# Kernel optimization log

Hardware: AMD Instinct MI355X
Metric: run time of the kernel (lower is better)

## Reference

```python
import jax, jax.numpy as jnp
import numpy as np

B, N, CIN, COUT = 2, 150000, 64, 64
SPATIAL = (128, 128, 128)  # spatial_shape forward arg, fixed here (list arg)
EPS = 1e-5


def setup_inputs() -> dict:
    key = jax.random.key(0)
    k1, k2, k3 = jax.random.split(key, 3)
    features = jax.random.normal(k1, (B, N, CIN), jnp.float32)
    coordinates = jax.random.randint(k2, (B, N, 3), 0, SPATIAL[0], jnp.int32)
    # SparseConv3d weight: 3x3x3 kernel flattened to 27 offsets, [27, Cin, Cout]
    weight = jax.random.normal(k3, (27, CIN, COUT), jnp.float32) * 0.05
    gamma = jnp.ones((COUT,), jnp.float32)
    beta = jnp.zeros((COUT,), jnp.float32)
    return {"features": features, "coordinates": coordinates, "weight": weight,
            "gamma": gamma, "beta": beta, "batch_size": B}


def _rulebook_ids(coordinates, batch_size):
    """For each of 27 kernel offsets, the flat input-point id feeding each output
    site (output sites = input sites, rulebook gather). Empty/OOB -> BN (zero row)."""
    X, Y, Z = SPATIAL
    Np = coordinates.shape[1]
    BN = batch_size * Np
    pid = jnp.arange(BN, dtype=jnp.int32)
    b = jnp.repeat(jnp.arange(batch_size, dtype=jnp.int32), Np)
    c = coordinates.reshape(-1, 3)
    # dense voxel hash: coord -> point id (max for deterministic collision handling)
    grid = jnp.full((batch_size, X, Y, Z), -1, jnp.int32)
    grid = grid.at[b, c[:, 0], c[:, 1], c[:, 2]].max(pid)
    # 27 offsets in {-1,0,1}^3 (padding=1, kernel=3, stride=1)
    r = jnp.arange(-1, 2, dtype=jnp.int32)
    offs = jnp.stack(jnp.meshgrid(r, r, r, indexing="ij"), -1).reshape(27, 3)
    nc = c[None, :, :] + offs[:, None, :]                      # [27, BN, 3]
    hi = jnp.array([X, Y, Z], jnp.int32)
    valid = jnp.all((nc >= 0) & (nc < hi), axis=-1)            # [27, BN]
    ncc = jnp.clip(nc, 0, hi - 1)
    ids = grid[b[None, :], ncc[..., 0], ncc[..., 1], ncc[..., 2]]
    return jnp.where(valid & (ids >= 0), ids, BN)              # BN -> zero row


def reference(features, coordinates, weight, gamma, beta, batch_size):
    Bs, Np, Cin = features.shape
    BN = Bs * Np
    ids = _rulebook_ids(coordinates, batch_size)               # [27, BN]
    feats = jnp.concatenate(
        [features.reshape(BN, Cin), jnp.zeros((1, Cin), features.dtype)], 0)

    # gather-GEMM-scatter accumulated over the 27 kernel offsets
    def step(acc, xs):
        idk, wk = xs
        return acc + feats[idk] @ wk, None

    out0 = jnp.zeros((BN, weight.shape[-1]), features.dtype)
    out, _ = jax.lax.scan(step, out0, (ids, weight))

    # BatchNorm1d (training stats over all points) + ReLU
    mean = out.mean(axis=0)
    var = out.var(axis=0)
    out = (out - mean) * jax.lax.rsqrt(var + EPS) * gamma + beta
    out = jax.nn.relu(out)
    return out.reshape(Bs, Np, -1)
```

## Files before the change

kernel.cpp:

```cpp
#include <hip/hip_runtime.h>

#define GS 128
#define GS3 (GS*GS*GS)
#define NPTS 150000
#define NBATCH 2
#define BN_TOT (NBATCH*NPTS)
#define CONV_BLOCKS 2344
#define BN_PAD (CONV_BLOCKS*128)
#define ZROW   BN_PAD
#define EPS 1e-5f
#define NBKT 8192

#define OFF_GRID   0ull
#define SZ_GRID    ((size_t)NBATCH*GS3*4)
#define OFF_WFRAG  (OFF_GRID + SZ_GRID)
#define SZ_WFRAG   ((size_t)27*4096*2)
#define OFF_STATS  (OFF_WFRAG + SZ_WFRAG)
#define OFF_CNT    (OFF_STATS + 512)
#define OFF_CUR    (OFF_CNT + NBKT*4)
#define OFF_SIDX   (OFF_CUR + NBKT*4)
#define OFF_CSORT  (OFF_SIDX + 1200128)
#define OFF_FB16S  (OFF_CSORT + (size_t)BN_PAD*16)
#define OFF_IDS    (OFF_FB16S + (size_t)(BN_PAD+1)*128)

typedef __attribute__((ext_vector_type(8))) short bf16x8;
typedef __attribute__((ext_vector_type(4))) float f32x4;
typedef unsigned int u32;
typedef const __attribute__((address_space(1))) u32* gas_u32p;
typedef __attribute__((address_space(3))) u32* las_u32p;

__device__ __forceinline__ short f2bf(float f) {
    union { float f; unsigned u; } v; v.f = f;
    unsigned rr = v.u + 0x7fffu + ((v.u >> 16) & 1u);
    return (short)(rr >> 16);
}

__global__ __launch_bounds__(256) void k_count(const int* __restrict__ coords,
                                               int* __restrict__ grid,
                                               u32* __restrict__ cnt) {
    int p = blockIdx.x*256 + threadIdx.x;
    if (p >= BN_TOT) return;
    int x = coords[p*3+0], y = coords[p*3+1], z = coords[p*3+2];
    int b = (p >= NPTS);
    atomicMax(&grid[(b<<21) | (x<<14) | (y<<7) | z], p);
    atomicAdd(&cnt[(b<<12) | ((x>>3)<<8) | ((y>>3)<<4) | (z>>3)], 1u);
}

__global__ __launch_bounds__(1024) void k_scan(const u32* __restrict__ cnt,
                                               u32* __restrict__ cur) {
    __shared__ u32 ps[1024];
    int t = threadIdx.x;
    u32 l[8]; u32 s = 0;
    #pragma unroll
    for (int i = 0; i < 8; ++i) { l[i] = cnt[t*8+i]; s += l[i]; }
    ps[t] = s; __syncthreads();
    for (int off = 1; off < 1024; off <<= 1) {
        u32 v = (t >= off) ? ps[t-off] : 0u; __syncthreads();
        ps[t] += v; __syncthreads();
    }
    u32 run = (t == 0) ? 0u : ps[t-1];
    #pragma unroll
    for (int i = 0; i < 8; ++i) { cur[t*8+i] = run; run += l[i]; }
}

__global__ __launch_bounds__(256) void k_place(const float* __restrict__ feats,
                                               const int* __restrict__ coords,
                                               u32* __restrict__ cur,
                                               int* __restrict__ sortidx,
                                               int4* __restrict__ csorted,
                                               ushort* __restrict__ fb16s) {
    int p = blockIdx.x*256 + threadIdx.x;
    if (p >= BN_PAD) return;
    if (p >= BN_TOT) { csorted[p] = make_int4(-9,-9,-9,0); return; }
    int x = coords[p*3+0], y = coords[p*3+1], z = coords[p*3+2];
    int b = (p >= NPTS);
    int bkt = (b<<12) | ((x>>3)<<8) | ((y>>3)<<4) | (z>>3);
    int pos = (int)atomicAdd(&cur[bkt], 1u);
    sortidx[p] = pos;
    csorted[pos] = make_int4(x, y, z, p);
    const float4* s = (const float4*)(feats + (size_t)p*64);
    ushort* d = fb16s + (size_t)pos*64;
    #pragma unroll
    for (int i = 0; i < 8; ++i) {
        float4 a = s[2*i], c = s[2*i+1];
        ushort4 u0 = { (ushort)f2bf(a.x),(ushort)f2bf(a.y),(ushort)f2bf(a.z),(ushort)f2bf(a.w) };
        ushort4 u1 = { (ushort)f2bf(c.x),(ushort)f2bf(c.y),(ushort)f2bf(c.z),(ushort)f2bf(c.w) };
        ((ushort4*)d)[2*i] = u0; ((ushort4*)d)[2*i+1] = u1;
    }
}

__global__ __launch_bounds__(256) void k_ids(const int4* __restrict__ csorted,
                                             const int* __restrict__ grid,
                                             const int* __restrict__ sortidx,
                                             int* __restrict__ ids) {
    int s = blockIdx.x*256 + threadIdx.x;
    if (s >= BN_PAD) return;
    int4 c = csorted[s];
    const bool pad = (s >= BN_TOT);
    const int gb = (c.w >= NPTS) ? GS3 : 0;
    #pragma unroll
    for (int k = 0; k < 27; ++k) {
        int dx = k/9 - 1, dy = (k/3)%3 - 1, dz = k%3 - 1;
        int nx = c.x+dx, ny = c.y+dy, nz = c.z+dz;
        int sid = ZROW;
        if (!pad && (((unsigned)nx < 128u) & ((unsigned)ny < 128u) &
                     ((unsigned)nz < 128u))) {
            int pid = grid[gb + (nx<<14) + (ny<<7) + nz];
            if (pid >= 0) sid = sortidx[pid];
        }
        ids[(size_t)k*BN_PAD + s] = sid;
    }
}

__global__ __launch_bounds__(256) void k_prefrag(const float* __restrict__ w,
                                                 short* __restrict__ wfrag) {
    int t = blockIdx.x * 256 + threadIdx.x;
    if (t >= 27*2*4*64*8) return;
    int i    = t & 7;
    int lane = (t >> 3) & 63;
    int tt   = (t >> 9) & 3;
    int c    = (t >> 11) & 1;
    int k    = t >> 12;
    int kk = c*32 + (lane >> 4)*8 + i;
    int co = tt*16 + (lane & 15);
    wfrag[t] = f2bf(w[(k*64 + kk)*64 + co]);
}

__global__ __launch_bounds__(256, 3) void k_conv(
    const ushort* __restrict__ fb16s,
    const int4* __restrict__ csorted,
    const int* __restrict__ ids_g,
    const ushort* __restrict__ wfrag,
    float* __restrict__ out,
    float* __restrict__ gstats)
{
    __shared__ __align__(16) ushort ldsB[2][4096];
    __shared__ int ids_lds[27*128];
    __shared__ float bsum[64], bsq[64];

    const int tid  = threadIdx.x;
    const int lane = tid & 63;
    const int wv   = tid >> 6;
    const int r    = lane & 15;
    const int seg  = lane >> 4;
    const int p0b  = blockIdx.x * 128;
    const int wrow = wv*32 + r;

    auto stage = [&](int kk, int bsel) {
        const u32* g = (const u32*)(wfrag + (size_t)kk*4096) + tid*4;
        u32* l  = (u32*)(&ldsB[bsel][wv*512]);
        __builtin_amdgcn_global_load_lds((gas_u32p)g,  (las_u32p)l,  16, 0, 0);
        const u32* g2 = g + 1024;
        u32* l2 = (u32*)(&ldsB[bsel][2048 + wv*512]);
        __builtin_amdgcn_global_load_lds((gas_u32p)g2, (las_u32p)l2, 16, 0, 0);
    };

#define LDA4(AC, sid0, sid1) {                                            \
        const ushort* a0_ = fb16s + (size_t)(sid0)*64 + seg*8;            \
        const ushort* a1_ = fb16s + (size_t)(sid1)*64 + seg*8;            \
        AC[0] = *(const bf16x8*)(a0_);  AC[1] = *(const bf16x8*)(a0_+32); \
        AC[2] = *(const bf16x8*)(a1_);  AC[3] = *(const bf16x8*)(a1_+32); }

    f32x4 t0q0={0,0,0,0}, t0q1={0,0,0,0}, t0q2={0,0,0,0}, t0q3={0,0,0,0};
    f32x4 t1q0={0,0,0,0}, t1q1={0,0,0,0}, t1q2={0,0,0,0}, t1q3={0,0,0,0};
    bf16x8 aE[4], aO[4];

    #pragma unroll
    for (int c = 0; c < 14; ++c) {
        int idx = c*256 + tid;
        if (idx < 27*128)
            ids_lds[idx] = ids_g[(size_t)(idx>>7)*BN_PAD + p0b + (idx&127)];
    }
    int i00 = ids_g[p0b + wrow];
    int i01 = ids_g[p0b + wrow + 16];
    int i10 = ids_g[(size_t)BN_PAD + p0b + wrow];
    int i11 = ids_g[(size_t)BN_PAD + p0b + wrow + 16];
    __syncthreads();
    __builtin_amdgcn_sched_barrier(0);
    LDA4(aE, i00, i01);
    __builtin_amdgcn_sched_barrier(0);
    stage(0, 0);
    __builtin_amdgcn_sched_barrier(0);
    LDA4(aO, i10, i11);
    __builtin_amdgcn_sched_barrier(0);

    auto phase = [&](int k, bf16x8 (&AC)[4], int bsel) {
        asm volatile("s_waitcnt vmcnt(4)" ::: "memory");
        __builtin_amdgcn_sched_barrier(0);
        __builtin_amdgcn_s_barrier();
        __builtin_amdgcn_sched_barrier(0);
        const bf16x8* bb = (const bf16x8*)ldsB[bsel];
        bf16x8 b0 = bb[0*64+lane], b1 = bb[1*64+lane],
               b2 = bb[2*64+lane], b3 = bb[3*64+lane],
               b4 = bb[4*64+lane], b5 = bb[5*64+lane],
               b6 = bb[6*64+lane], b7 = bb[7*64+lane];
        int kp2 = (k+2 > 26) ? 26 : k+2;
        int idn0 = ids_lds[kp2*128 + wrow];
        int idn1 = ids_lds[kp2*128 + wrow + 16];
        if (k < 26) stage(k+1, bsel^1);
        __builtin_amdgcn_sched_barrier(0);
        t0q0 = __builtin_amdgcn_mfma_f32_16x16x32_bf16(AC[0], b0, t0q0, 0,0,0);
        t0q1 = __builtin_amdgcn_mfma_f32_16x16x32_bf16(AC[0], b1, t0q1, 0,0,0);
        t0q2 = __builtin_amdgcn_mfma_f32_16x16x32_bf16(AC[0], b2, t0q2, 0,0,0);
        t0q3 = __builtin_amdgcn_mfma_f32_16x16x32_bf16(AC[0], b3, t0q3, 0,0,0);
        t0q0 = __builtin_amdgcn_mfma_f32_16x16x32_bf16(AC[1], b4, t0q0, 0,0,0);
        t0q1 = __builtin_amdgcn_mfma_f32_16x16x32_bf16(AC[1], b5, t0q1, 0,0,0);
        t0q2 = __builtin_amdgcn_mfma_f32_16x16x32_bf16(AC[1], b6, t0q2, 0,0,0);
        t0q3 = __builtin_amdgcn_mfma_f32_16x16x32_bf16(AC[1], b7, t0q3, 0,0,0);
        t1q0 = __builtin_amdgcn_mfma_f32_16x16x32_bf16(AC[2], b0, t1q0, 0,0,0);
        t1q1 = __builtin_amdgcn_mfma_f32_16x16x32_bf16(AC[2], b1, t1q1, 0,0,0);
        t1q2 = __builtin_amdgcn_mfma_f32_16x16x32_bf16(AC[2], b2, t1q2, 0,0,0);
        t1q3 = __builtin_amdgcn_mfma_f32_16x16x32_bf16(AC[2], b3, t1q3, 0,0,0);
        t1q0 = __builtin_amdgcn_mfma_f32_16x16x32_bf16(AC[3], b4, t1q0, 0,0,0);
        t1q1 = __builtin_amdgcn_mfma_f32_16x16x32_bf16(AC[3], b5, t1q1, 0,0,0);
        t1q2 = __builtin_amdgcn_mfma_f32_16x16x32_bf16(AC[3], b6, t1q2, 0,0,0);
        t1q3 = __builtin_amdgcn_mfma_f32_16x16x32_bf16(AC[3], b7, t1q3, 0,0,0);
        __builtin_amdgcn_sched_barrier(0);
        if (k < 26) { LDA4(AC, idn0, idn1); }
        __builtin_amdgcn_sched_barrier(0);
    };

    #pragma unroll 1
    for (int t = 0; t < 13; ++t) {
        phase(2*t,   aE, 0);
        phase(2*t+1, aO, 1);
    }
    phase(26, aE, 0);

    #pragma unroll
    for (int j = 0; j < 4; ++j) {
        int row0 = p0b + wv*32 + seg*4 + j;
        if (row0 < BN_TOT) {
            int opid = csorted[row0].w;
            float* ob = out + (size_t)opid*64 + r;
            ob[ 0] = t0q0[j]; ob[16] = t0q1[j]; ob[32] = t0q2[j]; ob[48] = t0q3[j];
        }
        int row1 = row0 + 16;
        if (row1 < BN_TOT) {
            int opid = csorted[row1].w;
            float* ob = out + (size_t)opid*64 + r;
            ob[ 0] = t1q0[j]; ob[16] = t1q1[j]; ob[32] = t1q2[j]; ob[48] = t1q3[j];
        }
    }

    if (tid < 64) { bsum[tid] = 0.f; bsq[tid] = 0.f; }
    __syncthreads();
    float s0=0,s1=0,s2=0,s3=0,q0=0,q1=0,q2=0,q3=0;
    #pragma unroll
    for (int j = 0; j < 4; ++j) {
        s0 += t0q0[j] + t1q0[j];  q0 += t0q0[j]*t0q0[j] + t1q0[j]*t1q0[j];
        s1 += t0q1[j] + t1q1[j];  q1 += t0q1[j]*t0q1[j] + t1q1[j]*t1q1[j];
        s2 += t0q2[j] + t1q2[j];  q2 += t0q2[j]*t0q2[j] + t1q2[j]*t1q2[j];
        s3 += t0q3[j] + t1q3[j];  q3 += t0q3[j]*t0q3[j] + t1q3[j]*t1q3[j];
    }
    atomicAdd(&bsum[ 0 + r], s0);  atomicAdd(&bsq[ 0 + r], q0);
    atomicAdd(&bsum[16 + r], s1);  atomicAdd(&bsq[16 + r], q1);
    atomicAdd(&bsum[32 + r], s2);  atomicAdd(&bsq[32 + r], q2);
    atomicAdd(&bsum[48 + r], s3);  atomicAdd(&bsq[48 + r], q3);
    __syncthreads();
    if (tid < 64) { atomicAdd(&gstats[tid], bsum[tid]); atomicAdd(&gstats[64+tid], bsq[tid]); }
#undef LDA4
}

__global__ __launch_bounds__(256) void k_norm(float* __restrict__ out,
                                              const float* __restrict__ stats,
                                              const float* __restrict__ gamma,
                                              const float* __restrict__ beta) {
    int i = blockIdx.x*256 + threadIdx.x;
    const int n4 = BN_TOT*16;
    if (i >= n4) return;
    float4 v = ((const float4*)out)[i];
    int ch = (i & 15) * 4;
    float o[4] = {v.x, v.y, v.z, v.w};
    float rp[4];
    #pragma unroll
    for (int j = 0; j < 4; ++j) {
        int c = ch + j;
        float mean = stats[c] * (1.f/BN_TOT);
        float var  = stats[64+c] * (1.f/BN_TOT) - mean*mean;
        float y = (o[j] - mean) * rsqrtf(var + EPS) * gamma[c] + beta[c];
        rp[j] = fmaxf(y, 0.f);
    }
    float4 rv; rv.x = rp[0]; rv.y = rp[1]; rv.z = rp[2]; rv.w = rp[3];
    ((float4*)out)[i] = rv;
}

extern "C" void kernel_launch(void* const* d_in, const int* in_sizes, int n_in,
                              void* d_out, int out_size, void* d_ws, size_t ws_size,
                              hipStream_t stream) {
    const float* feats  = (const float*)d_in[0];
    const int*   coords = (const int*)d_in[1];
    const float* weight = (const float*)d_in[2];
    const float* gamma  = (const float*)d_in[3];
    const float* beta   = (const float*)d_in[4];
    float* out = (float*)d_out;

    char*   ws      = (char*)d_ws;
    int*    grid    = (int*)(ws + OFF_GRID);
    short*  wfrag   = (short*)(ws + OFF_WFRAG);
    float*  stats   = (float*)(ws + OFF_STATS);
    u32*    cnt     = (u32*)(ws + OFF_CNT);
    u32*    cur     = (u32*)(ws + OFF_CUR);
    int*    sortidx = (int*)(ws + OFF_SIDX);
    int4*   csorted = (int4*)(ws + OFF_CSORT);
    ushort* fb16s   = (ushort*)(ws + OFF_FB16S);
    int*    idbuf   = (int*)(ws + OFF_IDS);

    hipMemsetAsync(grid,  0xFF, SZ_GRID, stream);
    hipMemsetAsync(stats, 0, 512, stream);
    hipMemsetAsync(cnt,   0, NBKT*4, stream);
    hipMemsetAsync(fb16s + (size_t)BN_TOT*64, 0,
                   (size_t)(BN_PAD + 1 - BN_TOT)*128, stream);

    k_count  <<<(BN_TOT + 255)/256, 256, 0, stream>>>(coords, grid, cnt);
    k_scan   <<<1, 1024, 0, stream>>>(cnt, cur);
    k_place  <<<(BN_PAD + 255)/256, 256, 0, stream>>>(feats, coords, cur,
                                                      sortidx, csorted, fb16s);
    k_ids    <<<(BN_PAD + 255)/256, 256, 0, stream>>>(csorted, grid, sortidx, idbuf);
    k_prefrag<<<(27*2*4*64*8)/256, 256, 0, stream>>>(weight, wfrag);
    k_conv   <<<CONV_BLOCKS, 256, 0, stream>>>(fb16s, csorted, idbuf,
                                               (const ushort*)wfrag, out, stats);
    k_norm   <<<(BN_TOT*16)/256, 256, 0, stream>>>(out, stats, gamma, beta);
}
```

Baseline: 270.4 us.

## Process kernel offsets in pairs per pipeline phase with zero-padded 28th offset

The conv main loop now handles two kernel offsets per phase, staging both weight slices into a doubled LDS buffer and prefetching eight feature vectors at a time. The offset count is padded to 28 with a zero weight slice and zero-row ids, so the loop runs 14 uniform phases without a tail. This halves the number of barriers and waitcnt points per block and deepens gather prefetch. In exchange it does one extra offset's wasted MFMA and gather work, doubles LDS and A-register usage, which may reduce occupancy.

```diff
diff --git a/kernel.cpp b/kernel.cpp
--- a/kernel.cpp
+++ b/kernel.cpp
@@ -10,11 +10,13 @@
 #define ZROW   BN_PAD
 #define EPS 1e-5f
 #define NBKT 8192
+#define NKS 28
+#define NPAIR 14
 
 #define OFF_GRID   0ull
 #define SZ_GRID    ((size_t)NBATCH*GS3*4)
 #define OFF_WFRAG  (OFF_GRID + SZ_GRID)
-#define SZ_WFRAG   ((size_t)27*4096*2)
+#define SZ_WFRAG   ((size_t)NKS*4096*2)
 #define OFF_STATS  (OFF_WFRAG + SZ_WFRAG)
 #define OFF_CNT    (OFF_STATS + 512)
 #define OFF_CUR    (OFF_CNT + NBKT*4)
@@ -110,17 +112,19 @@
         }
         ids[(size_t)k*BN_PAD + s] = sid;
     }
+    ids[(size_t)27*BN_PAD + s] = ZROW;
 }
 
 __global__ __launch_bounds__(256) void k_prefrag(const float* __restrict__ w,
                                                  short* __restrict__ wfrag) {
     int t = blockIdx.x * 256 + threadIdx.x;
-    if (t >= 27*2*4*64*8) return;
+    if (t >= NKS*4096) return;
     int i    = t & 7;
     int lane = (t >> 3) & 63;
     int tt   = (t >> 9) & 3;
     int c    = (t >> 11) & 1;
     int k    = t >> 12;
+    if (k >= 27) { wfrag[t] = 0; return; }
     int kk = c*32 + (lane >> 4)*8 + i;
     int co = tt*16 + (lane & 15);
     wfrag[t] = f2bf(w[(k*64 + kk)*64 + co]);
@@ -134,8 +138,8 @@
     float* __restrict__ out,
     float* __restrict__ gstats)
 {
-    __shared__ __align__(16) ushort ldsB[2][4096];
-    __shared__ int ids_lds[27*128];
+    __shared__ __align__(16) ushort ldsB[2][8192];
+    __shared__ int ids_lds[NKS*128];
     __shared__ float bsum[64], bsq[64];
 
     const int tid  = threadIdx.x;
@@ -146,58 +150,67 @@
     const int p0b  = blockIdx.x * 128;
     const int wrow = wv*32 + r;
 
-    auto stage = [&](int kk, int bsel) {
-        const u32* g = (const u32*)(wfrag + (size_t)kk*4096) + tid*4;
-        u32* l  = (u32*)(&ldsB[bsel][wv*512]);
-        __builtin_amdgcn_global_load_lds((gas_u32p)g,  (las_u32p)l,  16, 0, 0);
-        const u32* g2 = g + 1024;
-        u32* l2 = (u32*)(&ldsB[bsel][2048 + wv*512]);
-        __builtin_amdgcn_global_load_lds((gas_u32p)g2, (las_u32p)l2, 16, 0, 0);
+    auto stage = [&](int jp, int bsel) {
+        #pragma unroll
+        for (int c = 0; c < 4; ++c) {
+            int chunk = c*4 + wv;
+            const u32* g = (const u32*)(wfrag + (size_t)jp*8192 + chunk*512) + lane*4;
+            u32* l = (u32*)(&ldsB[bsel][chunk*512]);
+            __builtin_amdgcn_global_load_lds((gas_u32p)g, (las_u32p)l, 16, 0, 0);
+        }
     };
 
-#define LDA4(AC, sid0, sid1) {                                            \
-        const ushort* a0_ = fb16s + (size_t)(sid0)*64 + seg*8;            \
-        const ushort* a1_ = fb16s + (size_t)(sid1)*64 + seg*8;            \
-        AC[0] = *(const bf16x8*)(a0_);  AC[1] = *(const bf16x8*)(a0_+32); \
-        AC[2] = *(const bf16x8*)(a1_);  AC[3] = *(const bf16x8*)(a1_+32); }
+#define LDA8(AC, i00, i01, i10, i11) {                                   \
+        const ushort* q0_ = fb16s + (size_t)(i00)*64 + seg*8;            \
+        const ushort* q1_ = fb16s + (size_t)(i01)*64 + seg*8;            \
+        const ushort* q2_ = fb16s + (size_t)(i10)*64 + seg*8;            \
+        const ushort* q3_ = fb16s + (size_t)(i11)*64 + seg*8;            \
+        AC[0]=*(const bf16x8*)(q0_); AC[1]=*(const bf16x8*)(q0_+32);     \
+        AC[2]=*(const bf16x8*)(q1_); AC[3]=*(const bf16x8*)(q1_+32);     \
+        AC[4]=*(const bf16x8*)(q2_); AC[5]=*(const bf16x8*)(q2_+32);     \
+        AC[6]=*(const bf16x8*)(q3_); AC[7]=*(const bf16x8*)(q3_+32); }
 
     f32x4 t0q0={0,0,0,0}, t0q1={0,0,0,0}, t0q2={0,0,0,0}, t0q3={0,0,0,0};
     f32x4 t1q0={0,0,0,0}, t1q1={0,0,0,0}, t1q2={0,0,0,0}, t1q3={0,0,0,0};
-    bf16x8 aE[4], aO[4];
-
-    #pragma unroll
-    for (int c = 0; c < 14; ++c) {
+    bf16x8 aE[8], aO[8];
+
+    #pragma unroll
+    for (int c = 0; c < NKS/2; ++c) {
         int idx = c*256 + tid;
-        if (idx < 27*128)
-            ids_lds[idx] = ids_g[(size_t)(idx>>7)*BN_PAD + p0b + (idx&127)];
-    }
-    int i00 = ids_g[p0b + wrow];
-    int i01 = ids_g[p0b + wrow + 16];
-    int i10 = ids_g[(size_t)BN_PAD + p0b + wrow];
-    int i11 = ids_g[(size_t)BN_PAD + p0b + wrow + 16];
+        ids_lds[idx] = ids_g[(size_t)(idx>>7)*BN_PAD + p0b + (idx&127)];
+    }
+    int e00 = ids_g[(size_t)0*BN_PAD + p0b + wrow], e01 = ids_g[(size_t)0*BN_PAD + p0b + wrow + 16];
+    int e10 = ids_g[(size_t)1*BN_PAD + p0b + wrow], e11 = ids_g[(size_t)1*BN_PAD + p0b + wrow + 16];
+    int o00 = ids_g[(size_t)2*BN_PAD + p0b + wrow], o01 = ids_g[(size_t)2*BN_PAD + p0b + wrow + 16];
+    int o10 = ids_g[(size_t)3*BN_PAD + p0b + wrow], o11 = ids_g[(size_t)3*BN_PAD + p0b + wrow + 16];
     __syncthreads();
     __builtin_amdgcn_sched_barrier(0);
-    LDA4(aE, i00, i01);
+    LDA8(aE, e00, e01, e10, e11);
     __builtin_amdgcn_sched_barrier(0);
     stage(0, 0);
     __builtin_amdgcn_sched_barrier(0);
-    LDA4(aO, i10, i11);
+    LDA8(aO, o00, o01, o10, o11);
     __builtin_amdgcn_sched_barrier(0);
 
-    auto phase = [&](int k, bf16x8 (&AC)[4], int bsel) {
-        asm volatile("s_waitcnt vmcnt(4)" ::: "memory");
-        __builtin_amdgcn_sched_barrier(0);
+    auto phaseP = [&](int j, bf16x8 (&AC)[8]) {
+        asm volatile("s_waitcnt vmcnt(8)" ::: "memory");
         __builtin_amdgcn_s_barrier();
         __builtin_amdgcn_sched_barrier(0);
-        const bf16x8* bb = (const bf16x8*)ldsB[bsel];
-        bf16x8 b0 = bb[0*64+lane], b1 = bb[1*64+lane],
-               b2 = bb[2*64+lane], b3 = bb[3*64+lane],
-               b4 = bb[4*64+lane], b5 = bb[5*64+lane],
-               b6 = bb[6*64+lane], b7 = bb[7*64+lane];
-        int kp2 = (k+2 > 26) ? 26 : k+2;
-        int idn0 = ids_lds[kp2*128 + wrow];
-        int idn1 = ids_lds[kp2*128 + wrow + 16];
-        if (k < 26) stage(k+1, bsel^1);
+        const int bsel = j & 1;
+        const ushort* bb = ldsB[bsel];
+        bf16x8 b0 = *(const bf16x8*)(bb + 0*512 + lane*8);
+        bf16x8 b1 = *(const bf16x8*)(bb + 1*512 + lane*8);
+        bf16x8 b2 = *(const bf16x8*)(bb + 2*512 + lane*8);
+        bf16x8 b3 = *(const bf16x8*)(bb + 3*512 + lane*8);
+        bf16x8 b4 = *(const bf16x8*)(bb + 4*512 + lane*8);
+        bf16x8 b5 = *(const bf16x8*)(bb + 5*512 + lane*8);
+        bf16x8 b6 = *(const bf16x8*)(bb + 6*512 + lane*8);
+        bf16x8 b7 = *(const bf16x8*)(bb + 7*512 + lane*8);
+        int jp2 = (j+2 > NPAIR-1) ? NPAIR-1 : j+2;
+        int n00 = ids_lds[(2*jp2  )*128 + wrow], n01 = ids_lds[(2*jp2  )*128 + wrow + 16];
+        int n10 = ids_lds[(2*jp2+1)*128 + wrow], n11 = ids_lds[(2*jp2+1)*128 + wrow + 16];
+        int jp1 = (j+1 > NPAIR-1) ? NPAIR-1 : j+1;
+        stage(jp1, bsel^1);
         __builtin_amdgcn_sched_barrier(0);
         t0q0 = __builtin_amdgcn_mfma_f32_16x16x32_bf16(AC[0], b0, t0q0, 0,0,0);
         t0q1 = __builtin_amdgcn_mfma_f32_16x16x32_bf16(AC[0], b1, t0q1, 0,0,0);
@@ -215,17 +228,40 @@
         t1q1 = __builtin_amdgcn_mfma_f32_16x16x32_bf16(AC[3], b5, t1q1, 0,0,0);
         t1q2 = __builtin_amdgcn_mfma_f32_16x16x32_bf16(AC[3], b6, t1q2, 0,0,0);
         t1q3 = __builtin_amdgcn_mfma_f32_16x16x32_bf16(AC[3], b7, t1q3, 0,0,0);
+        b0 = *(const bf16x8*)(bb + 4096 + 0*512 + lane*8);
+        b1 = *(const bf16x8*)(bb + 4096 + 1*512 + lane*8);
+        b2 = *(const bf16x8*)(bb + 4096 + 2*512 + lane*8);
+        b3 = *(const bf16x8*)(bb + 4096 + 3*512 + lane*8);
+        b4 = *(const bf16x8*)(bb + 4096 + 4*512 + lane*8);
+        b5 = *(const bf16x8*)(bb + 4096 + 5*512 + lane*8);
+        b6 = *(const bf16x8*)(bb + 4096 + 6*512 + lane*8);
+        b7 = *(const bf16x8*)(bb + 4096 + 7*512 + lane*8);
+        t0q0 = __builtin_amdgcn_mfma_f32_16x16x32_bf16(AC[4], b0, t0q0, 0,0,0);
+        t0q1 = __builtin_amdgcn_mfma_f32_16x16x32_bf16(AC[4], b1, t0q1, 0,0,0);
+        t0q2 = __builtin_amdgcn_mfma_f32_16x16x32_bf16(AC[4], b2, t0q2, 0,0,0);
+        t0q3 = __builtin_amdgcn_mfma_f32_16x16x32_bf16(AC[4], b3, t0q3, 0,0,0);
+        t0q0 = __builtin_amdgcn_mfma_f32_16x16x32_bf16(AC[5], b4, t0q0, 0,0,0);
+        t0q1 = __builtin_amdgcn_mfma_f32_16x16x32_bf16(AC[5], b5, t0q1, 0,0,0);
+        t0q2 = __builtin_amdgcn_mfma_f32_16x16x32_bf16(AC[5], b6, t0q2, 0,0,0);
+        t0q3 = __builtin_amdgcn_mfma_f32_16x16x32_bf16(AC[5], b7, t0q3, 0,0,0);
+        t1q0 = __builtin_amdgcn_mfma_f32_16x16x32_bf16(AC[6], b0, t1q0, 0,0,0);
+        t1q1 = __builtin_amdgcn_mfma_f32_16x16x32_bf16(AC[6], b1, t1q1, 0,0,0);
+        t1q2 = __builtin_amdgcn_mfma_f32_16x16x32_bf16(AC[6], b2, t1q2, 0,0,0);
+        t1q3 = __builtin_amdgcn_mfma_f32_16x16x32_bf16(AC[6], b3, t1q3, 0,0,0);
+        t1q0 = __builtin_amdgcn_mfma_f32_16x16x32_bf16(AC[7], b4, t1q0, 0,0,0);
+        t1q1 = __builtin_amdgcn_mfma_f32_16x16x32_bf16(AC[7], b5, t1q1, 0,0,0);
+        t1q2 = __builtin_amdgcn_mfma_f32_16x16x32_bf16(AC[7], b6, t1q2, 0,0,0);
+        t1q3 = __builtin_amdgcn_mfma_f32_16x16x32_bf16(AC[7], b7, t1q3, 0,0,0);
         __builtin_amdgcn_sched_barrier(0);
-        if (k < 26) { LDA4(AC, idn0, idn1); }
+        LDA8(AC, n00, n01, n10, n11);
         __builtin_amdgcn_sched_barrier(0);
     };
 
     #pragma unroll 1
-    for (int t = 0; t < 13; ++t) {
-        phase(2*t,   aE, 0);
-        phase(2*t+1, aO, 1);
-    }
-    phase(26, aE, 0);
+    for (int t = 0; t < 7; ++t) {
+        phaseP(2*t,   aE);
+        phaseP(2*t+1, aO);
+    }
 
     #pragma unroll
     for (int j = 0; j < 4; ++j) {
@@ -259,7 +295,7 @@
     atomicAdd(&bsum[48 + r], s3);  atomicAdd(&bsq[48 + r], q3);
     __syncthreads();
     if (tid < 64) { atomicAdd(&gstats[tid], bsum[tid]); atomicAdd(&gstats[64+tid], bsq[tid]); }
-#undef LDA4
+#undef LDA8
 }
 
 __global__ __launch_bounds__(256) void k_norm(float* __restrict__ out,
@@ -317,7 +353,7 @@
     k_place  <<<(BN_PAD + 255)/256, 256, 0, stream>>>(feats, coords, cur,
                                                       sortidx, csorted, fb16s);
     k_ids    <<<(BN_PAD + 255)/256, 256, 0, stream>>>(csorted, grid, sortidx, idbuf);
-    k_prefrag<<<(27*2*4*64*8)/256, 256, 0, stream>>>(weight, wfrag);
+    k_prefrag<<<(NKS*4096)/256, 256, 0, stream>>>(weight, wfrag);
     k_conv   <<<CONV_BLOCKS, 256, 0, stream>>>(fb16s, csorted, idbuf,
                                                (const ushort*)wfrag, out, stats);
     k_norm   <<<(BN_TOT*16)/256, 256, 0, stream>>>(out, stats, gamma, beta);
```

Result: no change. 272.1 us (+0.6%).

## Compact rulebook to skip empty neighbor offsets and accumulate in LDS

Applied to the files above, without the earlier changes.

Replaces the dense 27xN id table with per-block compacted rule entries that list only valid (neighbor, row) pairs, built with ballot/popcount prefix sums. The conv kernel processes only those entries in 16-row MFMA tiles and scatter-accumulates results into a shared-memory output tile with LDS atomics. Blocks grow to 256 output rows and weight fragments are read straight from global memory instead of double-buffered through LDS. This removes the MFMA and gather work for empty neighbors, which are the large majority at this density, but adds LDS atomic traffic, lower occupancy from the 68KB LDS tile, and uncoalesced weight loads.

```diff
diff --git a/kernel.cpp b/kernel.cpp
--- a/kernel.cpp
+++ b/kernel.cpp
@@ -5,11 +5,12 @@
 #define NPTS 150000
 #define NBATCH 2
 #define BN_TOT (NBATCH*NPTS)
-#define CONV_BLOCKS 2344
-#define BN_PAD (CONV_BLOCKS*128)
+#define CONV_BLOCKS 1172
+#define BN_PAD (CONV_BLOCKS*256)
 #define ZROW   BN_PAD
 #define EPS 1e-5f
 #define NBKT 8192
+#define EB   6912
 
 #define OFF_GRID   0ull
 #define SZ_GRID    ((size_t)NBATCH*GS3*4)
@@ -21,13 +22,12 @@
 #define OFF_SIDX   (OFF_CUR + NBKT*4)
 #define OFF_CSORT  (OFF_SIDX + 1200128)
 #define OFF_FB16S  (OFF_CSORT + (size_t)BN_PAD*16)
-#define OFF_IDS    (OFF_FB16S + (size_t)(BN_PAD+1)*128)
+#define OFF_ENT    (OFF_FB16S + (size_t)(BN_PAD+1)*128)
+#define OFF_CNTS   (OFF_ENT + (size_t)CONV_BLOCKS*EB*4)
 
 typedef __attribute__((ext_vector_type(8))) short bf16x8;
 typedef __attribute__((ext_vector_type(4))) float f32x4;
 typedef unsigned int u32;
-typedef const __attribute__((address_space(1))) u32* gas_u32p;
-typedef __attribute__((address_space(3))) u32* las_u32p;
 
 __device__ __forceinline__ short f2bf(float f) {
     union { float f; unsigned u; } v; v.f = f;
@@ -89,33 +89,58 @@
     }
 }
 
-__global__ __launch_bounds__(256) void k_ids(const int4* __restrict__ csorted,
-                                             const int* __restrict__ grid,
-                                             const int* __restrict__ sortidx,
-                                             int* __restrict__ ids) {
-    int s = blockIdx.x*256 + threadIdx.x;
-    if (s >= BN_PAD) return;
+__global__ __launch_bounds__(256) void k_rules(const int4* __restrict__ csorted,
+                                               const int* __restrict__ grid,
+                                               const int* __restrict__ sortidx,
+                                               int* __restrict__ entries,
+                                               int* __restrict__ cnts) {
+    __shared__ u32 wcnt[4];
+    __shared__ u32 basev;
+    const int tid = threadIdx.x, lane = tid & 63, wv = tid >> 6;
+    const int blk = blockIdx.x;
+    const int row = tid;
+    const int s = blk*256 + row;
     int4 c = csorted[s];
     const bool pad = (s >= BN_TOT);
     const int gb = (c.w >= NPTS) ? GS3 : 0;
+
+    int sid[27];
     #pragma unroll
     for (int k = 0; k < 27; ++k) {
         int dx = k/9 - 1, dy = (k/3)%3 - 1, dz = k%3 - 1;
         int nx = c.x+dx, ny = c.y+dy, nz = c.z+dz;
-        int sid = ZROW;
-        if (!pad && (((unsigned)nx < 128u) & ((unsigned)ny < 128u) &
-                     ((unsigned)nz < 128u))) {
-            int pid = grid[gb + (nx<<14) + (ny<<7) + nz];
-            if (pid >= 0) sid = sortidx[pid];
-        }
-        ids[(size_t)k*BN_PAD + s] = sid;
+        int ok = (int)(!pad & ((unsigned)nx < 128u) & ((unsigned)ny < 128u) &
+                       ((unsigned)nz < 128u));
+        int pid = grid[gb + ((nx&127)<<14) + ((ny&127)<<7) + (nz&127)];
+        pid = ok ? pid : -1;
+        int sv = sortidx[pid < 0 ? 0 : pid];
+        sid[k] = (pid >= 0) ? sv : ZROW;
+    }
+
+    if (tid == 0) basev = 0;
+    int* eb = entries + (size_t)blk * EB;
+    __syncthreads();
+    #pragma unroll 1
+    for (int k = 0; k < 27; ++k) {
+        bool pred = (sid[k] != ZROW);
+        unsigned long long b = __ballot(pred);
+        if (lane == 0) wcnt[wv] = (u32)__popcll(b);
+        __syncthreads();
+        u32 off = basev;
+        u32 w0 = wcnt[0], w1 = wcnt[1], w2 = wcnt[2], w3 = wcnt[3];
+        u32 woff = (wv > 0 ? w0 : 0u) + (wv > 1 ? w1 : 0u) + (wv > 2 ? w2 : 0u);
+        u32 tot = w0 + w1 + w2 + w3;
+        u32 lc = (u32)__popcll(b & ((1ull << lane) - 1ull));
+        if (pred) eb[off + woff + lc] = (sid[k] << 8) | row;
+        __syncthreads();
+        if (tid == 0) { basev = off + tot; cnts[blk*32 + k] = (int)tot; }
     }
 }
 
 __global__ __launch_bounds__(256) void k_prefrag(const float* __restrict__ w,
                                                  short* __restrict__ wfrag) {
     int t = blockIdx.x * 256 + threadIdx.x;
-    if (t >= 27*2*4*64*8) return;
+    if (t >= 27*4096) return;
     int i    = t & 7;
     int lane = (t >> 3) & 63;
     int tt   = (t >> 9) & 3;
@@ -126,16 +151,17 @@
     wfrag[t] = f2bf(w[(k*64 + kk)*64 + co]);
 }
 
-__global__ __launch_bounds__(256, 3) void k_conv(
+__global__ __launch_bounds__(256, 2) void k_conv(
     const ushort* __restrict__ fb16s,
     const int4* __restrict__ csorted,
-    const int* __restrict__ ids_g,
+    const int* __restrict__ entries,
+    const int* __restrict__ cnts,
     const ushort* __restrict__ wfrag,
     float* __restrict__ out,
     float* __restrict__ gstats)
 {
-    __shared__ __align__(16) ushort ldsB[2][4096];
-    __shared__ int ids_lds[27*128];
+    __shared__ float oacc[256*68];
+    __shared__ int   cl[27];
     __shared__ float bsum[64], bsq[64];
 
     const int tid  = threadIdx.x;
@@ -143,123 +169,90 @@
     const int wv   = tid >> 6;
     const int r    = lane & 15;
     const int seg  = lane >> 4;
-    const int p0b  = blockIdx.x * 128;
-    const int wrow = wv*32 + r;
-
-    auto stage = [&](int kk, int bsel) {
-        const u32* g = (const u32*)(wfrag + (size_t)kk*4096) + tid*4;
-        u32* l  = (u32*)(&ldsB[bsel][wv*512]);
-        __builtin_amdgcn_global_load_lds((gas_u32p)g,  (las_u32p)l,  16, 0, 0);
-        const u32* g2 = g + 1024;
-        u32* l2 = (u32*)(&ldsB[bsel][2048 + wv*512]);
-        __builtin_amdgcn_global_load_lds((gas_u32p)g2, (las_u32p)l2, 16, 0, 0);
-    };
-
-#define LDA4(AC, sid0, sid1) {                                            \
-        const ushort* a0_ = fb16s + (size_t)(sid0)*64 + seg*8;            \
-        const ushort* a1_ = fb16s + (size_t)(sid1)*64 + seg*8;            \
-        AC[0] = *(const bf16x8*)(a0_);  AC[1] = *(const bf16x8*)(a0_+32); \
-        AC[2] = *(const bf16x8*)(a1_);  AC[3] = *(const bf16x8*)(a1_+32); }
-
-    f32x4 t0q0={0,0,0,0}, t0q1={0,0,0,0}, t0q2={0,0,0,0}, t0q3={0,0,0,0};
-    f32x4 t1q0={0,0,0,0}, t1q1={0,0,0,0}, t1q2={0,0,0,0}, t1q3={0,0,0,0};
-    bf16x8 aE[4], aO[4];
-
-    #pragma unroll
-    for (int c = 0; c < 14; ++c) {
-        int idx = c*256 + tid;
-        if (idx < 27*128)
-            ids_lds[idx] = ids_g[(size_t)(idx>>7)*BN_PAD + p0b + (idx&127)];
-    }
-    int i00 = ids_g[p0b + wrow];
-    int i01 = ids_g[p0b + wrow + 16];
-    int i10 = ids_g[(size_t)BN_PAD + p0b + wrow];
-    int i11 = ids_g[(size_t)BN_PAD + p0b + wrow + 16];
-    __syncthreads();
-    __builtin_amdgcn_sched_barrier(0);
-    LDA4(aE, i00, i01);
-    __builtin_amdgcn_sched_barrier(0);
-    stage(0, 0);
-    __builtin_amdgcn_sched_barrier(0);
-    LDA4(aO, i10, i11);
-    __builtin_amdgcn_sched_barrier(0);
-
-    auto phase = [&](int k, bf16x8 (&AC)[4], int bsel) {
-        asm volatile("s_waitcnt vmcnt(4)" ::: "memory");
-        __builtin_amdgcn_sched_barrier(0);
-        __builtin_amdgcn_s_barrier();
-        __builtin_amdgcn_sched_barrier(0);
-        const bf16x8* bb = (const bf16x8*)ldsB[bsel];
-        bf16x8 b0 = bb[0*64+lane], b1 = bb[1*64+lane],
-               b2 = bb[2*64+lane], b3 = bb[3*64+lane],
-               b4 = bb[4*64+lane], b5 = bb[5*64+lane],
-               b6 = bb[6*64+lane], b7 = bb[7*64+lane];
-        int kp2 = (k+2 > 26) ? 26 : k+2;
-        int idn0 = ids_lds[kp2*128 + wrow];
-        int idn1 = ids_lds[kp2*128 + wrow + 16];
-        if (k < 26) stage(k+1, bsel^1);
-        __builtin_amdgcn_sched_barrier(0);
-        t0q0 = __builtin_amdgcn_mfma_f32_16x16x32_bf16(AC[0], b0, t0q0, 0,0,0);
-        t0q1 = __builtin_amdgcn_mfma_f32_16x16x32_bf16(AC[0], b1, t0q1, 0,0,0);
-        t0q2 = __builtin_amdgcn_mfma_f32_16x16x32_bf16(AC[0], b2, t0q2, 0,0,0);
-        t0q3 = __builtin_amdgcn_mfma_f32_16x16x32_bf16(AC[0], b3, t0q3, 0,0,0);
-        t0q0 = __builtin_amdgcn_mfma_f32_16x16x32_bf16(AC[1], b4, t0q0, 0,0,0);
-        t0q1 = __builtin_amdgcn_mfma_f32_16x16x32_bf16(AC[1], b5, t0q1, 0,0,0);
-        t0q2 = __builtin_amdgcn_mfma_f32_16x16x32_bf16(AC[1], b6, t0q2, 0,0,0);
-        t0q3 = __builtin_amdgcn_mfma_f32_16x16x32_bf16(AC[1], b7, t0q3, 0,0,0);
-        t1q0 = __builtin_amdgcn_mfma_f32_16x16x32_bf16(AC[2], b0, t1q0, 0,0,0);
-        t1q1 = __builtin_amdgcn_mfma_f32_16x16x32_bf16(AC[2], b1, t1q1, 0,0,0);
-        t1q2 = __builtin_amdgcn_mfma_f32_16x16x32_bf16(AC[2], b2, t1q2, 0,0,0);
-        t1q3 = __builtin_amdgcn_mfma_f32_16x16x32_bf16(AC[2], b3, t1q3, 0,0,0);
-        t1q0 = __builtin_amdgcn_mfma_f32_16x16x32_bf16(AC[3], b4, t1q0, 0,0,0);
-        t1q1 = __builtin_amdgcn_mfma_f32_16x16x32_bf16(AC[3], b5, t1q1, 0,0,0);
-        t1q2 = __builtin_amdgcn_mfma_f32_16x16x32_bf16(AC[3], b6, t1q2, 0,0,0);
-        t1q3 = __builtin_amdgcn_mfma_f32_16x16x32_bf16(AC[3], b7, t1q3, 0,0,0);
-        __builtin_amdgcn_sched_barrier(0);
-        if (k < 26) { LDA4(AC, idn0, idn1); }
-        __builtin_amdgcn_sched_barrier(0);
-    };
-
-    #pragma unroll 1
-    for (int t = 0; t < 13; ++t) {
-        phase(2*t,   aE, 0);
-        phase(2*t+1, aO, 1);
-    }
-    phase(26, aE, 0);
-
-    #pragma unroll
-    for (int j = 0; j < 4; ++j) {
-        int row0 = p0b + wv*32 + seg*4 + j;
-        if (row0 < BN_TOT) {
-            int opid = csorted[row0].w;
-            float* ob = out + (size_t)opid*64 + r;
-            ob[ 0] = t0q0[j]; ob[16] = t0q1[j]; ob[32] = t0q2[j]; ob[48] = t0q3[j];
-        }
-        int row1 = row0 + 16;
-        if (row1 < BN_TOT) {
-            int opid = csorted[row1].w;
-            float* ob = out + (size_t)opid*64 + r;
-            ob[ 0] = t1q0[j]; ob[16] = t1q1[j]; ob[32] = t1q2[j]; ob[48] = t1q3[j];
-        }
-    }
-
+    const int blk  = blockIdx.x;
+    const int p0b  = blk * 256;
+
+    #pragma unroll
+    for (int i = 0; i < 68; ++i) oacc[i*256 + tid] = 0.f;
+    if (tid < 27) cl[tid] = cnts[blk*32 + tid];
     if (tid < 64) { bsum[tid] = 0.f; bsq[tid] = 0.f; }
     __syncthreads();
-    float s0=0,s1=0,s2=0,s3=0,q0=0,q1=0,q2=0,q3=0;
-    #pragma unroll
-    for (int j = 0; j < 4; ++j) {
-        s0 += t0q0[j] + t1q0[j];  q0 += t0q0[j]*t0q0[j] + t1q0[j]*t1q0[j];
-        s1 += t0q1[j] + t1q1[j];  q1 += t0q1[j]*t0q1[j] + t1q1[j]*t1q1[j];
-        s2 += t0q2[j] + t1q2[j];  q2 += t0q2[j]*t0q2[j] + t1q2[j]*t1q2[j];
-        s3 += t0q3[j] + t1q3[j];  q3 += t0q3[j]*t0q3[j] + t1q3[j]*t1q3[j];
-    }
-    atomicAdd(&bsum[ 0 + r], s0);  atomicAdd(&bsq[ 0 + r], q0);
-    atomicAdd(&bsum[16 + r], s1);  atomicAdd(&bsq[16 + r], q1);
-    atomicAdd(&bsum[32 + r], s2);  atomicAdd(&bsq[32 + r], q2);
-    atomicAdd(&bsum[48 + r], s3);  atomicAdd(&bsq[48 + r], q3);
+
+    const int* eb = entries + (size_t)blk * EB;
+    const bf16x8* wfp = (const bf16x8*)wfrag;
+
+    int ebase = 0, tbase = 0;
+    #pragma unroll 1
+    for (int k = 0; k < 27; ++k) {
+        const int cnt = cl[k];
+        const int nt = (cnt + 15) >> 4;
+        const bf16x8* wb = wfp + (size_t)k*512;
+        int t = (wv - tbase) & 3;
+        for (; t < nt; t += 4) {
+            int ei = t*16 + r;
+            int pe = eb[ebase + (ei < cnt ? ei : cnt-1)];
+            if (ei >= cnt) pe = (ZROW << 8);
+            int sid = pe >> 8;
+            const ushort* ap = fb16s + (size_t)sid*64 + seg*8;
+            bf16x8 a0 = *(const bf16x8*)(ap);
+            bf16x8 a1 = *(const bf16x8*)(ap + 32);
+            bf16x8 b0 = wb[0*64+lane], b1 = wb[1*64+lane],
+                   b2 = wb[2*64+lane], b3 = wb[3*64+lane],
+                   b4 = wb[4*64+lane], b5 = wb[5*64+lane],
+                   b6 = wb[6*64+lane], b7 = wb[7*64+lane];
+            f32x4 q0 = {0,0,0,0}, q1 = {0,0,0,0}, q2 = {0,0,0,0}, q3 = {0,0,0,0};
+            q0 = __builtin_amdgcn_mfma_f32_16x16x32_bf16(a0, b0, q0, 0,0,0);
+            q1 = __builtin_amdgcn_mfma_f32_16x16x32_bf16(a0, b1, q1, 0,0,0);
+            q2 = __builtin_amdgcn_mfma_f32_16x16x32_bf16(a0, b2, q2, 0,0,0);
+            q3 = __builtin_amdgcn_mfma_f32_16x16x32_bf16(a0, b3, q3, 0,0,0);
+            q0 = __builtin_amdgcn_mfma_f32_16x16x32_bf16(a1, b4, q0, 0,0,0);
+            q1 = __builtin_amdgcn_mfma_f32_16x16x32_bf16(a1, b5, q1, 0,0,0);
+            q2 = __builtin_amdgcn_mfma_f32_16x16x32_bf16(a1, b6, q2, 0,0,0);
+            q3 = __builtin_amdgcn_mfma_f32_16x16x32_bf16(a1, b7, q3, 0,0,0);
+            #pragma unroll
+            for (int j = 0; j < 4; ++j) {
+                int rw = __shfl(pe, seg*4 + j, 64) & 0xFF;
+                float* dst = &oacc[rw*68 + r];
+                atomicAdd(dst +  0, q0[j]);
+                atomicAdd(dst + 16, q1[j]);
+                atomicAdd(dst + 32, q2[j]);
+                atomicAdd(dst + 48, q3[j]);
+            }
+        }
+        ebase += cnt; tbase += nt;
+    }
+    __syncthreads();
+
+    const int rg = tid >> 2, c4 = tid & 3;
+    float s[16], sq[16];
+    #pragma unroll
+    for (int i = 0; i < 16; ++i) { s[i] = 0.f; sq[i] = 0.f; }
+    #pragma unroll
+    for (int p = 0; p < 4; ++p) {
+        int row = p*64 + rg;
+        const float* src = &oacc[row*68 + c4*16];
+        float4 v0 = *(const float4*)(src +  0);
+        float4 v1 = *(const float4*)(src +  4);
+        float4 v2 = *(const float4*)(src +  8);
+        float4 v3 = *(const float4*)(src + 12);
+        const float vv[16] = { v0.x,v0.y,v0.z,v0.w, v1.x,v1.y,v1.z,v1.w,
+                               v2.x,v2.y,v2.z,v2.w, v3.x,v3.y,v3.z,v3.w };
+        #pragma unroll
+        for (int i = 0; i < 16; ++i) { s[i] += vv[i]; sq[i] += vv[i]*vv[i]; }
+        int srow = p0b + row;
+        if (srow < BN_TOT) {
+            int opid = csorted[srow].w;
+            float4* ob = (float4*)(out + (size_t)opid*64 + c4*16);
+            ob[0] = v0; ob[1] = v1; ob[2] = v2; ob[3] = v3;
+        }
+    }
+    #pragma unroll
+    for (int i = 0; i < 16; ++i) {
+        atomicAdd(&bsum[c4*16 + i], s[i]);
+        atomicAdd(&bsq [c4*16 + i], sq[i]);
+    }
     __syncthreads();
     if (tid < 64) { atomicAdd(&gstats[tid], bsum[tid]); atomicAdd(&gstats[64+tid], bsq[tid]); }
-#undef LDA4
 }
 
 __global__ __launch_bounds__(256) void k_norm(float* __restrict__ out,
@@ -304,7 +297,8 @@
     int*    sortidx = (int*)(ws + OFF_SIDX);
     int4*   csorted = (int4*)(ws + OFF_CSORT);
     ushort* fb16s   = (ushort*)(ws + OFF_FB16S);
-    int*    idbuf   = (int*)(ws + OFF_IDS);
+    int*    entries = (int*)(ws + OFF_ENT);
+    int*    cnts    = (int*)(ws + OFF_CNTS);
 
     hipMemsetAsync(grid,  0xFF, SZ_GRID, stream);
     hipMemsetAsync(stats, 0, 512, stream);
@@ -316,9 +310,10 @@
     k_scan   <<<1, 1024, 0, stream>>>(cnt, cur);
     k_place  <<<(BN_PAD + 255)/256, 256, 0, stream>>>(feats, coords, cur,
                                                       sortidx, csorted, fb16s);
-    k_ids    <<<(BN_PAD + 255)/256, 256, 0, stream>>>(csorted, grid, sortidx, idbuf);
-    k_prefrag<<<(27*2*4*64*8)/256, 256, 0, stream>>>(weight, wfrag);
-    k_conv   <<<CONV_BLOCKS, 256, 0, stream>>>(fb16s, csorted, idbuf,
+    k_rules  <<<CONV_BLOCKS, 256, 0, stream>>>(csorted, grid, sortidx,
+                                               entries, cnts);
+    k_prefrag<<<(27*4096)/256, 256, 0, stream>>>(weight, wfrag);
+    k_conv   <<<CONV_BLOCKS, 256, 0, stream>>>(fb16s, csorted, entries, cnts,
                                                (const ushort*)wfrag, out, stats);
     k_norm   <<<(BN_TOT*16)/256, 256, 0, stream>>>(out, stats, gamma, beta);
 }
```

New measurement: 584.1 us. 2.16x slower.
